# Optimization experiments

Measured on AMD Instinct MI355X. Metric: run time of the kernel, lower is better.

## Reference

```python
import jax, jax.numpy as jnp
import numpy as np

WINDOW_SIZE = 11
VAL_RANGE = 1.0
N_CHANNEL = 3
MS_WEIGHTS = jnp.array([0.0448, 0.2856, 0.3001, 0.2363, 0.1333], dtype=jnp.float32)


def _gaussian_window(window_size, sigma, channel):
    x = jnp.arange(window_size, dtype=jnp.float32)
    g = jnp.exp(-((x - window_size // 2) ** 2) / (2.0 * sigma ** 2))
    g = g / jnp.sum(g)
    w2d = jnp.outer(g, g)  # [ws, ws]
    # depthwise kernel in OIHW with feature_group_count=channel: [C, 1, ws, ws]
    return jnp.broadcast_to(w2d[None, None], (channel, 1, window_size, window_size))


def _dwconv(x, kernel):
    # x: [B, C, H, W], kernel: [C, 1, ws, ws], valid padding, groups=C
    return jax.lax.conv_general_dilated(
        x, kernel, window_strides=(1, 1), padding='VALID',
        dimension_numbers=('NCHW', 'OIHW', 'NCHW'),
        feature_group_count=kernel.shape[0])


def _avg_pool2(x):
    # kernel 2, stride 2, no padding (floor mode)
    s = jax.lax.reduce_window(x, 0.0, jax.lax.add,
                              (1, 1, 2, 2), (1, 1, 2, 2), 'VALID')
    return s * 0.25


def setup_inputs() -> dict:
    key = jax.random.key(0)
    k1, k2 = jax.random.split(key)
    output = jax.random.uniform(k1, (16, 3, 512, 512), dtype=jnp.float32)
    target = jax.random.uniform(k2, (16, 3, 512, 512), dtype=jnp.float32)
    return {"output": output, "target": target}


def reference(output, target):
    window = _gaussian_window(WINDOW_SIZE, 1.5, N_CHANNEL)
    L = VAL_RANGE
    C1 = (0.01 * L) ** 2
    C2 = (0.03 * L) ** 2
    cs_list, ssim_list = [], []
    for _ in range(MS_WEIGHTS.shape[0]):
        mu1 = _dwconv(output, window)
        mu2 = _dwconv(target, window)
        sigma1_sq = _dwconv(output * output, window) - mu1 * mu1
        sigma2_sq = _dwconv(target * target, window) - mu2 * mu2
        sigma12 = _dwconv(output * target, window) - mu1 * mu2
        denom = sigma1_sq + sigma2_sq + C2
        cs = (2.0 * sigma12 + C2) / denom
        ssim = (2.0 * mu1 * mu2 + C1) * (2.0 * sigma12 + C2) / (
            (mu1 * mu1 + mu2 * mu2 + C1) * denom)
        cs_list.append(jax.nn.relu(jnp.mean(cs)))
        ssim_list.append(jax.nn.relu(jnp.mean(ssim)))
        output = _avg_pool2(output)
        target = _avg_pool2(target)
    cs = (jnp.stack(cs_list) + 1.0) / 2.0
    ssim = (jnp.stack(ssim_list) + 1.0) / 2.0
    ms_ssim = jnp.prod((cs ** MS_WEIGHTS)[:-1]) * (ssim ** MS_WEIGHTS)[-1]
    return 1.0 - ms_ssim
```

## Files before the change

### kernel.cpp

```cpp
#include <hip/hip_runtime.h>

#define HALO 10
#define NIMG 48

#define GWLIST { 0.0010284f, 0.0075987f, 0.0360008f, 0.1093607f, 0.2130056f, \
                 0.2660117f, 0.2130056f, 0.1093607f, 0.0360008f, 0.0075987f, 0.0010284f }

#define PP   56
#define PSZ  (48 * 56)
#define HT0  (2 * PSZ)
#define HTP  56
#define HTSZ (32 * 56)
#define WT0  (HT0 + 5 * HTSZ)
#define LDSH (WT0 + 64 * 8)

typedef _Float16 half8 __attribute__((ext_vector_type(8)));
typedef _Float16 half4 __attribute__((ext_vector_type(4)));
typedef float    floatx4 __attribute__((ext_vector_type(4)));

template <bool FUSE>
__global__ __launch_bounds__(256, 5) void ssim_mfma_kernel(
    const float* __restrict__ A, const float* __restrict__ B,
    int H, int W, float2* __restrict__ partial,
    float* __restrict__ poolA, float* __restrict__ poolB)
{
    __shared__ __align__(16) _Float16 sm[LDSH];
    __shared__ float red[16];

    const float w[11] = GWLIST;
    const int tid  = threadIdx.x;
    const int lane = tid & 63;
    const int wv   = tid >> 6;
    const int gx0  = blockIdx.x * 32;
    const int gy0  = blockIdx.y * 32;
    const int z    = blockIdx.z;
    const float* a = A + (size_t)z * H * W;
    const float* b = B + (size_t)z * H * W;

    if (tid < 64) {
        int base = ((tid >> 4) << 3) - (tid & 15);
        half8 wf;
        #pragma unroll
        for (int i = 0; i < 8; ++i) {
            int j = base + i;
            float v = 0.f;
            #pragma unroll
            for (int J = 0; J < 11; ++J) v = (j == J) ? w[J] : v;
            wf[i] = (_Float16)v;
        }
        *(half8*)&sm[WT0 + tid * 8] = wf;
    }

    const bool fast = (gy0 + 48 <= H) && (gx0 + 48 <= W);
    for (int e = tid; e < 288; e += 256) {
        int r = e / 6, c8 = e - r * 6;
        float fa[8], fb[8];
        if (fast) {
            const float* pa = a + (size_t)(gy0 + r) * W + gx0 + c8 * 8;
            const float* pb = b + (size_t)(gy0 + r) * W + gx0 + c8 * 8;
            *(float4*)&fa[0] = *(const float4*)pa;
            *(float4*)&fa[4] = *(const float4*)(pa + 4);
            *(float4*)&fb[0] = *(const float4*)pb;
            *(float4*)&fb[4] = *(const float4*)(pb + 4);
        } else {
            int gy = gy0 + r;
            #pragma unroll
            for (int i = 0; i < 8; ++i) {
                int gx = gx0 + c8 * 8 + i;
                bool ok = (gy < H) && (gx < W);
                size_t idx = (size_t)gy * W + gx;
                fa[i] = ok ? a[idx] : 0.f;
                fb[i] = ok ? b[idx] : 0.f;
            }
        }
        half8 ha, hb;
        #pragma unroll
        for (int i = 0; i < 8; ++i) {
            ha[i] = (_Float16)fa[i];
            hb[i] = (_Float16)fb[i];
        }
        int o = r * PP + c8 * 8;
        *(half8*)&sm[o]       = ha;
        *(half8*)&sm[o + PSZ] = hb;
    }
    __syncthreads();

    const half8 wfrag = *(const half8*)&sm[WT0 + lane * 8];

    {
        const int arow = (lane & 15) * PP + ((lane >> 4) << 3);
        const int crow = (lane & 15) * HTP + ((lane >> 4) << 2);
        #pragma unroll 2
        for (int p = wv; p < 6; p += 4) {
            int m0 = (p >> 1) << 4;
            int x0 = (p & 1) << 4;
            int fb_ = m0 * PP + x0 + arow;
            half8 ha  = *(const half8*)&sm[fb_];
            half8 hb  = *(const half8*)&sm[fb_ + PSZ];
            half8 faa = ha * ha;
            half8 fbb = hb * hb;
            half8 fab = ha * hb;
            floatx4 zero = {0.f, 0.f, 0.f, 0.f};
            floatx4 c0 = __builtin_amdgcn_mfma_f32_16x16x32_f16(ha,  wfrag, zero, 0, 0, 0);
            floatx4 c1 = __builtin_amdgcn_mfma_f32_16x16x32_f16(hb,  wfrag, zero, 0, 0, 0);
            floatx4 c2 = __builtin_amdgcn_mfma_f32_16x16x32_f16(faa, wfrag, zero, 0, 0, 0);
            floatx4 c3 = __builtin_amdgcn_mfma_f32_16x16x32_f16(fbb, wfrag, zero, 0, 0, 0);
            floatx4 c4 = __builtin_amdgcn_mfma_f32_16x16x32_f16(fab, wfrag, zero, 0, 0, 0);
            int cb = HT0 + x0 * HTP + m0 + crow;
            half4 h0, h1, h2, h3, h4;
            #pragma unroll
            for (int i = 0; i < 4; ++i) {
                h0[i] = (_Float16)c0[i];
                h1[i] = (_Float16)c1[i];
                h2[i] = (_Float16)c2[i];
                h3[i] = (_Float16)c3[i];
                h4[i] = (_Float16)c4[i];
            }
            *(half4*)&sm[cb + 0 * HTSZ] = h0;
            *(half4*)&sm[cb + 1 * HTSZ] = h1;
            *(half4*)&sm[cb + 2 * HTSZ] = h2;
            *(half4*)&sm[cb + 3 * HTSZ] = h3;
            *(half4*)&sm[cb + 4 * HTSZ] = h4;
        }
    }
    __syncthreads();

    float csSum = 0.f, ssimSum = 0.f;
    {
        const int y0 = (wv >> 1) << 4;
        const int x0 = (wv & 1) << 4;
        const int brow = (lane & 15) * HTP + ((lane >> 4) << 3);
        floatx4 m[5];
        #pragma unroll
        for (int q = 0; q < 5; ++q) {
            half8 bfrag = *(const half8*)&sm[HT0 + q * HTSZ + x0 * HTP + y0 + brow];
            floatx4 c = {0.f, 0.f, 0.f, 0.f};
            m[q] = __builtin_amdgcn_mfma_f32_16x16x32_f16(wfrag, bfrag, c, 0, 0, 0);
        }
        const int OH = H - HALO, OW = W - HALO;
        const int gx  = gx0 + x0 + (lane & 15);
        const int gyb = gy0 + y0 + ((lane >> 4) << 2);
        const float C1 = 1e-4f;
        const float C2 = 9e-4f;
        if (gx < OW) {
            #pragma unroll
            for (int i = 0; i < 4; ++i) {
                int gy = gyb + i;
                if (gy < OH) {
                    float mu1 = m[0][i], mu2 = m[1][i];
                    float s1sq = m[2][i] - mu1 * mu1;
                    float s2sq = m[3][i] - mu2 * mu2;
                    float s12  = m[4][i] - mu1 * mu2;
                    float denom = s1sq + s2sq + C2;
                    float num   = 2.f * s12 + C2;
                    float csv = num * __frcp_rn(denom);
                    float ssv = csv * (2.f * mu1 * mu2 + C1) *
                                __frcp_rn(mu1 * mu1 + mu2 * mu2 + C1);
                    csSum   += csv;
                    ssimSum += ssv;
                }
            }
        }
    }

    #pragma unroll
    for (int off = 32; off > 0; off >>= 1) {
        csSum   += __shfl_down(csSum, off, 64);
        ssimSum += __shfl_down(ssimSum, off, 64);
    }
    if (lane == 0) {
        red[wv]     = csSum;
        red[8 + wv] = ssimSum;
    }
    __syncthreads();
    if (tid == 0) {
        float c = 0.f, s = 0.f;
        #pragma unroll
        for (int i = 0; i < 4; ++i) { c += red[i]; s += red[8 + i]; }
        int slot = (z * gridDim.y + blockIdx.y) * gridDim.x + blockIdx.x;
        partial[slot] = make_float2(c, s);
    }

    if (FUSE && tid < 128) {
        const int OH2 = H >> 1, OW2 = W >> 1;
        const int img = tid >> 6;
        const int rem = tid & 63;
        const int pr  = rem >> 2;
        const int pq  = rem & 3;
        const float* src = img ? b : a;
        float* dst = (img ? poolB : poolA) + (size_t)z * OH2 * OW2;
        size_t base = (size_t)(gy0 + 2 * pr) * W + gx0 + pq * 8;
        float4 r0 = *(const float4*)(src + base);
        float4 r1 = *(const float4*)(src + base + 4);
        float4 r2 = *(const float4*)(src + base + W);
        float4 r3 = *(const float4*)(src + base + W + 4);
        float4 o;
        o.x = 0.25f * (r0.x + r0.y + r2.x + r2.y);
        o.y = 0.25f * (r0.z + r0.w + r2.z + r2.w);
        o.z = 0.25f * (r1.x + r1.y + r3.x + r3.y);
        o.w = 0.25f * (r1.z + r1.w + r3.z + r3.w);
        *(float4*)(dst + (size_t)((gy0 >> 1) + pr) * OW2 + (gx0 >> 1) + pq * 4) = o;
    }
}

#define TH   32
#define ROWS (TH + HALO)
#define HSTR 32
#define HQ   (ROWS * HSTR)

template <bool FUSE>
__global__ __launch_bounds__(256, 5) void ssim_scalar_kernel(
    const float* __restrict__ A, const float* __restrict__ B,
    int H, int W, float2* __restrict__ partial,
    float* __restrict__ poolA, float* __restrict__ poolB)
{
    __shared__ __align__(16) float lds[5 * HQ];
    __shared__ float red[16];

    const float w[11] = GWLIST;

    const int tid = threadIdx.x;
    const int gx0 = blockIdx.x * 32;
    const int gy0 = blockIdx.y * TH;
    const int z   = blockIdx.z;
    const float* a = A + (size_t)z * H * W;
    const float* b = B + (size_t)z * H * W;

    const bool fast = (gy0 + ROWS <= H) && (gx0 + 44 <= W);
    for (int e = tid; e < ROWS * 8; e += 256) {
        int r = e >> 3, c0 = (e & 7) * 4;
        int gy = gy0 + r;
        float s1[4]  = {0.f, 0.f, 0.f, 0.f};
        float s2[4]  = {0.f, 0.f, 0.f, 0.f};
        float s11[4] = {0.f, 0.f, 0.f, 0.f};
        float s22[4] = {0.f, 0.f, 0.f, 0.f};
        float s12[4] = {0.f, 0.f, 0.f, 0.f};
        #pragma unroll
        for (int c = 0; c < 4; ++c) {
            float ea[4], eb[4];
            if (fast) {
                const float* pa = a + (size_t)gy * W + gx0 + c0 + 4 * c;
                const float* pb = b + (size_t)gy * W + gx0 + c0 + 4 * c;
                *(float4*)&ea[0] = *(const float4*)pa;
                *(float4*)&eb[0] = *(const float4*)pb;
            } else {
                #pragma unroll
                for (int t = 0; t < 4; ++t) {
                    int gx = gx0 + c0 + 4 * c + t;
                    bool ok = (gy < H) && (gx < W);
                    size_t idx = (size_t)gy * W + gx;
                    ea[t] = ok ? a[idx] : 0.f;
                    eb[t] = ok ? b[idx] : 0.f;
                }
            }
            #pragma unroll
            for (int mm = 0; mm < 4; ++mm) {
                const int i = 4 * c + mm;
                float va = ea[mm], vb = eb[mm];
                float vaa = va * va, vbb = vb * vb, vab = va * vb;
                #pragma unroll
                for (int k = 0; k < 4; ++k) {
                    const int j = i - k;
                    if (j >= 0 && j <= 10) {
                        float wj = w[j];
                        s1[k]  += wj * va;
                        s2[k]  += wj * vb;
                        s11[k] += wj * vaa;
                        s22[k] += wj * vbb;
                        s12[k] += wj * vab;
                    }
                }
            }
        }
        int hb = r * HSTR + c0;
        *(float4*)&lds[hb + 0 * HQ] = make_float4(s1[0],  s1[1],  s1[2],  s1[3]);
        *(float4*)&lds[hb + 1 * HQ] = make_float4(s2[0],  s2[1],  s2[2],  s2[3]);
        *(float4*)&lds[hb + 2 * HQ] = make_float4(s11[0], s11[1], s11[2], s11[3]);
        *(float4*)&lds[hb + 3 * HQ] = make_float4(s22[0], s22[1], s22[2], s22[3]);
        *(float4*)&lds[hb + 4 * HQ] = make_float4(s12[0], s12[1], s12[2], s12[3]);
    }
    __syncthreads();

    const float C1 = 1e-4f;
    const float C2 = 9e-4f;
    float csSum = 0.f, ssimSum = 0.f;
    {
        const int ox  = tid & 31;
        const int oy0 = (tid >> 5) * 4;
        float m[5][4];
        #pragma unroll
        for (int q = 0; q < 5; ++q) {
            const float* hq = &lds[q * HQ + oy0 * HSTR + ox];
            float win[14];
            #pragma unroll
            for (int i = 0; i < 14; ++i) win[i] = hq[i * HSTR];
            #pragma unroll
            for (int k = 0; k < 4; ++k) {
                float acc = 0.f;
                #pragma unroll
                for (int j = 0; j < 11; ++j) acc += w[j] * win[k + j];
                m[q][k] = acc;
            }
        }
        const int OH = H - HALO, OW = W - HALO;
        const int gx = gx0 + ox;
        #pragma unroll
        for (int k = 0; k < 4; ++k) {
            int gy = gy0 + oy0 + k;
            if (gy < OH && gx < OW) {
                float mu1 = m[0][k], mu2 = m[1][k];
                float s1sq = m[2][k] - mu1 * mu1;
                float s2sq = m[3][k] - mu2 * mu2;
                float s12  = m[4][k] - mu1 * mu2;
                float denom  = s1sq + s2sq + C2;
                float num_cs = 2.f * s12 + C2;
                float csv = num_cs * __frcp_rn(denom);
                float ssv = csv * (2.f * mu1 * mu2 + C1) *
                            __frcp_rn(mu1 * mu1 + mu2 * mu2 + C1);
                csSum   += csv;
                ssimSum += ssv;
            }
        }
    }

    #pragma unroll
    for (int off = 32; off > 0; off >>= 1) {
        csSum   += __shfl_down(csSum, off, 64);
        ssimSum += __shfl_down(ssimSum, off, 64);
    }
    int wave = tid >> 6, lane = tid & 63;
    if (lane == 0) {
        red[wave]     = csSum;
        red[8 + wave] = ssimSum;
    }
    __syncthreads();
    if (tid == 0) {
        float c = 0.f, s = 0.f;
        #pragma unroll
        for (int i = 0; i < 4; ++i) { c += red[i]; s += red[8 + i]; }
        int slot = (z * gridDim.y + blockIdx.y) * gridDim.x + blockIdx.x;
        partial[slot] = make_float2(c, s);
    }

    if (FUSE && tid < 128) {
        const int OH2 = H >> 1, OW2 = W >> 1;
        const int img = tid >> 6;
        const int rem = tid & 63;
        const int pr  = rem >> 2;
        const int pq  = rem & 3;
        const float* src = img ? b : a;
        float* dst = (img ? poolB : poolA) + (size_t)z * OH2 * OW2;
        size_t base = (size_t)(gy0 + 2 * pr) * W + gx0 + pq * 8;
        float4 r0 = *(const float4*)(src + base);
        float4 r1 = *(const float4*)(src + base + 4);
        float4 r2 = *(const float4*)(src + base + W);
        float4 r3 = *(const float4*)(src + base + W + 4);
        float4 o;
        o.x = 0.25f * (r0.x + r0.y + r2.x + r2.y);
        o.y = 0.25f * (r0.z + r0.w + r2.z + r2.w);
        o.z = 0.25f * (r1.x + r1.y + r3.x + r3.y);
        o.w = 0.25f * (r1.z + r1.w + r3.z + r3.w);
        *(float4*)(dst + (size_t)((gy0 >> 1) + pr) * OW2 + (gx0 >> 1) + pq * 4) = o;
    }
}

__global__ void final_kernel(const float2* __restrict__ partial, float* __restrict__ out) {
    __shared__ double red[8];
    __shared__ double resC[5], resS[5];
    const int segs[6] = {0, 12288, 15360, 16128, 16320, 16368};
    const int tid = threadIdx.x;
    for (int s = 0; s < 5; ++s) {
        double c = 0.0, v = 0.0;
        #pragma unroll 4
        for (int i = segs[s] + tid; i < segs[s + 1]; i += 256) {
            float2 p = partial[i];
            c += (double)p.x;
            v += (double)p.y;
        }
        #pragma unroll
        for (int off = 32; off > 0; off >>= 1) {
            c += __shfl_down(c, off, 64);
            v += __shfl_down(v, off, 64);
        }
        int wave = tid >> 6, lane = tid & 63;
        __syncthreads();
        if (lane == 0) { red[wave] = c; red[4 + wave] = v; }
        __syncthreads();
        if (tid == 0) {
            resC[s] = red[0] + red[1] + red[2] + red[3];
            resS[s] = red[4] + red[5] + red[6] + red[7];
        }
    }
    __syncthreads();
    if (tid == 0) {
        const double wgt[5] = {0.0448, 0.2856, 0.3001, 0.2363, 0.1333};
        double ms = 1.0;
        for (int s = 0; s < 5; ++s) {
            int Hs = 512 >> s;
            double cnt = (double)NIMG * (double)(Hs - 10) * (double)(Hs - 10);
            double cs = resC[s] / cnt;
            double sv = resS[s] / cnt;
            if (cs < 0.0) cs = 0.0;
            if (sv < 0.0) sv = 0.0;
            cs = (cs + 1.0) * 0.5;
            sv = (sv + 1.0) * 0.5;
            ms *= pow((s < 4) ? cs : sv, wgt[s]);
        }
        out[0] = (float)(1.0 - ms);
    }
}

extern "C" void kernel_launch(void* const* d_in, const int* in_sizes, int n_in,
                              void* d_out, int out_size, void* d_ws, size_t ws_size,
                              hipStream_t stream) {
    (void)in_sizes; (void)n_in; (void)out_size; (void)ws_size;
    const float* A0 = (const float*)d_in[0];
    const float* B0 = (const float*)d_in[1];
    float* out = (float*)d_out;

    char* ws = (char*)d_ws;
    float2* partial = (float2*)ws;
    float* pyr = (float*)(ws + (1 << 18));

    float* pa[5] = {nullptr, nullptr, nullptr, nullptr, nullptr};
    float* pb[5] = {nullptr, nullptr, nullptr, nullptr, nullptr};
    size_t off = 0;
    for (int s = 1; s <= 4; ++s) {
        int Hs = 512 >> s;
        size_t n = (size_t)NIMG * Hs * Hs;
        pa[s] = pyr + off; off += n;
        pb[s] = pyr + off; off += n;
    }

    const int segs[5] = {0, 12288, 15360, 16128, 16320};

    const float* curA = A0;
    const float* curB = B0;
    for (int s = 0; s < 5; ++s) {
        int Hs = 512 >> s;
        int g  = Hs >> 5;
        dim3 grid(g, g, NIMG);
        if (s < 2) {
            ssim_mfma_kernel<true><<<grid, 256, 0, stream>>>(
                curA, curB, Hs, Hs, partial + segs[s], pa[s + 1], pb[s + 1]);
            curA = pa[s + 1];
            curB = pb[s + 1];
        } else if (s < 4) {
            ssim_scalar_kernel<true><<<grid, 256, 0, stream>>>(
                curA, curB, Hs, Hs, partial + segs[s], pa[s + 1], pb[s + 1]);
            curA = pa[s + 1];
            curB = pb[s + 1];
        } else {
            ssim_scalar_kernel<false><<<grid, 256, 0, stream>>>(
                curA, curB, Hs, Hs, partial + segs[s], nullptr, nullptr);
        }
    }

    final_kernel<<<1, 256, 0, stream>>>(partial, out);
}
```

Baseline: 208.7 us.

## Process two tiles per block and prefetch second tile during first compute

```diff
diff --git a/kernel.cpp b/kernel.cpp
--- a/kernel.cpp
+++ b/kernel.cpp
@@ -18,151 +18,140 @@
 typedef _Float16 half4 __attribute__((ext_vector_type(4)));
 typedef float    floatx4 __attribute__((ext_vector_type(4)));
 
-template <bool FUSE>
-__global__ __launch_bounds__(256, 5) void ssim_mfma_kernel(
-    const float* __restrict__ A, const float* __restrict__ B,
-    int H, int W, float2* __restrict__ partial,
-    float* __restrict__ poolA, float* __restrict__ poolB)
-{
-    __shared__ __align__(16) _Float16 sm[LDSH];
-    __shared__ float red[16];
-
-    const float w[11] = GWLIST;
-    const int tid  = threadIdx.x;
-    const int lane = tid & 63;
-    const int wv   = tid >> 6;
-    const int gx0  = blockIdx.x * 32;
-    const int gy0  = blockIdx.y * 32;
-    const int z    = blockIdx.z;
-    const float* a = A + (size_t)z * H * W;
-    const float* b = B + (size_t)z * H * W;
-
-    if (tid < 64) {
-        int base = ((tid >> 4) << 3) - (tid & 15);
-        half8 wf;
+struct JR { float4 al, ah, bl, bh; };
+
+__device__ __forceinline__ void issue_job(const float* __restrict__ a,
+                                          const float* __restrict__ b,
+                                          int H, int W, int gx0, int gy0,
+                                          int e, bool fast, JR& r)
+{
+    int rr = e / 6, c8 = e - rr * 6;
+    if (fast) {
+        const float* pa = a + (size_t)(gy0 + rr) * W + gx0 + c8 * 8;
+        const float* pb = b + (size_t)(gy0 + rr) * W + gx0 + c8 * 8;
+        r.al = *(const float4*)pa;       r.ah = *(const float4*)(pa + 4);
+        r.bl = *(const float4*)pb;       r.bh = *(const float4*)(pb + 4);
+    } else {
+        float fa[8], fb[8];
+        int gy = gy0 + rr;
         #pragma unroll
         for (int i = 0; i < 8; ++i) {
-            int j = base + i;
-            float v = 0.f;
-            #pragma unroll
-            for (int J = 0; J < 11; ++J) v = (j == J) ? w[J] : v;
-            wf[i] = (_Float16)v;
-        }
-        *(half8*)&sm[WT0 + tid * 8] = wf;
-    }
-
-    const bool fast = (gy0 + 48 <= H) && (gx0 + 48 <= W);
-    for (int e = tid; e < 288; e += 256) {
-        int r = e / 6, c8 = e - r * 6;
-        float fa[8], fb[8];
-        if (fast) {
-            const float* pa = a + (size_t)(gy0 + r) * W + gx0 + c8 * 8;
-            const float* pb = b + (size_t)(gy0 + r) * W + gx0 + c8 * 8;
-            *(float4*)&fa[0] = *(const float4*)pa;
-            *(float4*)&fa[4] = *(const float4*)(pa + 4);
-            *(float4*)&fb[0] = *(const float4*)pb;
-            *(float4*)&fb[4] = *(const float4*)(pb + 4);
-        } else {
-            int gy = gy0 + r;
-            #pragma unroll
-            for (int i = 0; i < 8; ++i) {
-                int gx = gx0 + c8 * 8 + i;
-                bool ok = (gy < H) && (gx < W);
-                size_t idx = (size_t)gy * W + gx;
-                fa[i] = ok ? a[idx] : 0.f;
-                fb[i] = ok ? b[idx] : 0.f;
+            int gx = gx0 + c8 * 8 + i;
+            bool ok = (gy < H) && (gx < W);
+            size_t idx = (size_t)gy * W + gx;
+            fa[i] = ok ? a[idx] : 0.f;
+            fb[i] = ok ? b[idx] : 0.f;
+        }
+        r.al = make_float4(fa[0], fa[1], fa[2], fa[3]);
+        r.ah = make_float4(fa[4], fa[5], fa[6], fa[7]);
+        r.bl = make_float4(fb[0], fb[1], fb[2], fb[3]);
+        r.bh = make_float4(fb[4], fb[5], fb[6], fb[7]);
+    }
+}
+
+__device__ __forceinline__ void store_job(_Float16* __restrict__ sm, int e, const JR& r)
+{
+    int rr = e / 6, c8 = e - rr * 6;
+    float fa[8] = {r.al.x, r.al.y, r.al.z, r.al.w, r.ah.x, r.ah.y, r.ah.z, r.ah.w};
+    float fb[8] = {r.bl.x, r.bl.y, r.bl.z, r.bl.w, r.bh.x, r.bh.y, r.bh.z, r.bh.w};
+    half8 ha, hb;
+    #pragma unroll
+    for (int i = 0; i < 8; ++i) {
+        ha[i] = (_Float16)fa[i];
+        hb[i] = (_Float16)fb[i];
+    }
+    int o = rr * PP + c8 * 8;
+    *(half8*)&sm[o]       = ha;
+    *(half8*)&sm[o + PSZ] = hb;
+}
+
+__device__ __forceinline__ void stage2(_Float16* __restrict__ sm, half8 wfrag,
+                                       int lane, int wv)
+{
+    const int arow = (lane & 15) * PP + ((lane >> 4) << 3);
+    const int crow = (lane & 15) * HTP + ((lane >> 4) << 2);
+    #pragma unroll 2
+    for (int p = wv; p < 6; p += 4) {
+        int m0 = (p >> 1) << 4;
+        int x0 = (p & 1) << 4;
+        int fb_ = m0 * PP + x0 + arow;
+        half8 ha  = *(const half8*)&sm[fb_];
+        half8 hb  = *(const half8*)&sm[fb_ + PSZ];
+        half8 faa = ha * ha;
+        half8 fbb = hb * hb;
+        half8 fab = ha * hb;
+        floatx4 zero = {0.f, 0.f, 0.f, 0.f};
+        floatx4 c0 = __builtin_amdgcn_mfma_f32_16x16x32_f16(ha,  wfrag, zero, 0, 0, 0);
+        floatx4 c1 = __builtin_amdgcn_mfma_f32_16x16x32_f16(hb,  wfrag, zero, 0, 0, 0);
+        floatx4 c2 = __builtin_amdgcn_mfma_f32_16x16x32_f16(faa, wfrag, zero, 0, 0, 0);
+        floatx4 c3 = __builtin_amdgcn_mfma_f32_16x16x32_f16(fbb, wfrag, zero, 0, 0, 0);
+        floatx4 c4 = __builtin_amdgcn_mfma_f32_16x16x32_f16(fab, wfrag, zero, 0, 0, 0);
+        int cb = HT0 + x0 * HTP + m0 + crow;
+        half4 h0, h1, h2, h3, h4;
+        #pragma unroll
+        for (int i = 0; i < 4; ++i) {
+            h0[i] = (_Float16)c0[i];
+            h1[i] = (_Float16)c1[i];
+            h2[i] = (_Float16)c2[i];
+            h3[i] = (_Float16)c3[i];
+            h4[i] = (_Float16)c4[i];
+        }
+        *(half4*)&sm[cb + 0 * HTSZ] = h0;
+        *(half4*)&sm[cb + 1 * HTSZ] = h1;
+        *(half4*)&sm[cb + 2 * HTSZ] = h2;
+        *(half4*)&sm[cb + 3 * HTSZ] = h3;
+        *(half4*)&sm[cb + 4 * HTSZ] = h4;
+    }
+}
+
+__device__ __forceinline__ void stage3(const _Float16* __restrict__ sm, half8 wfrag,
+                                       int lane, int wv, int H, int W,
+                                       int gx0, int gy0,
+                                       float& csSum, float& ssimSum)
+{
+    const int y0 = (wv >> 1) << 4;
+    const int x0 = (wv & 1) << 4;
+    const int brow = (lane & 15) * HTP + ((lane >> 4) << 3);
+    floatx4 m[5];
+    #pragma unroll
+    for (int q = 0; q < 5; ++q) {
+        half8 bfrag = *(const half8*)&sm[HT0 + q * HTSZ + x0 * HTP + y0 + brow];
+        floatx4 c = {0.f, 0.f, 0.f, 0.f};
+        m[q] = __builtin_amdgcn_mfma_f32_16x16x32_f16(wfrag, bfrag, c, 0, 0, 0);
+    }
+    const int OH = H - HALO, OW = W - HALO;
+    const int gx  = gx0 + x0 + (lane & 15);
+    const int gyb = gy0 + y0 + ((lane >> 4) << 2);
+    const float C1 = 1e-4f;
+    const float C2 = 9e-4f;
+    csSum = 0.f; ssimSum = 0.f;
+    if (gx < OW) {
+        #pragma unroll
+        for (int i = 0; i < 4; ++i) {
+            int gy = gyb + i;
+            if (gy < OH) {
+                float mu1 = m[0][i], mu2 = m[1][i];
+                float s1sq = m[2][i] - mu1 * mu1;
+                float s2sq = m[3][i] - mu2 * mu2;
+                float s12  = m[4][i] - mu1 * mu2;
+                float denom = s1sq + s2sq + C2;
+                float num   = 2.f * s12 + C2;
+                float csv = num * __frcp_rn(denom);
+                float ssv = csv * (2.f * mu1 * mu2 + C1) *
+                            __frcp_rn(mu1 * mu1 + mu2 * mu2 + C1);
+                csSum   += csv;
+                ssimSum += ssv;
             }
         }
-        half8 ha, hb;
-        #pragma unroll
-        for (int i = 0; i < 8; ++i) {
-            ha[i] = (_Float16)fa[i];
-            hb[i] = (_Float16)fb[i];
-        }
-        int o = r * PP + c8 * 8;
-        *(half8*)&sm[o]       = ha;
-        *(half8*)&sm[o + PSZ] = hb;
-    }
-    __syncthreads();
-
-    const half8 wfrag = *(const half8*)&sm[WT0 + lane * 8];
-
-    {
-        const int arow = (lane & 15) * PP + ((lane >> 4) << 3);
-        const int crow = (lane & 15) * HTP + ((lane >> 4) << 2);
-        #pragma unroll 2
-        for (int p = wv; p < 6; p += 4) {
-            int m0 = (p >> 1) << 4;
-            int x0 = (p & 1) << 4;
-            int fb_ = m0 * PP + x0 + arow;
-            half8 ha  = *(const half8*)&sm[fb_];
-            half8 hb  = *(const half8*)&sm[fb_ + PSZ];
-            half8 faa = ha * ha;
-            half8 fbb = hb * hb;
-            half8 fab = ha * hb;
-            floatx4 zero = {0.f, 0.f, 0.f, 0.f};
-            floatx4 c0 = __builtin_amdgcn_mfma_f32_16x16x32_f16(ha,  wfrag, zero, 0, 0, 0);
-            floatx4 c1 = __builtin_amdgcn_mfma_f32_16x16x32_f16(hb,  wfrag, zero, 0, 0, 0);
-            floatx4 c2 = __builtin_amdgcn_mfma_f32_16x16x32_f16(faa, wfrag, zero, 0, 0, 0);
-            floatx4 c3 = __builtin_amdgcn_mfma_f32_16x16x32_f16(fbb, wfrag, zero, 0, 0, 0);
-            floatx4 c4 = __builtin_amdgcn_mfma_f32_16x16x32_f16(fab, wfrag, zero, 0, 0, 0);
-            int cb = HT0 + x0 * HTP + m0 + crow;
-            half4 h0, h1, h2, h3, h4;
-            #pragma unroll
-            for (int i = 0; i < 4; ++i) {
-                h0[i] = (_Float16)c0[i];
-                h1[i] = (_Float16)c1[i];
-                h2[i] = (_Float16)c2[i];
-                h3[i] = (_Float16)c3[i];
-                h4[i] = (_Float16)c4[i];
-            }
-            *(half4*)&sm[cb + 0 * HTSZ] = h0;
-            *(half4*)&sm[cb + 1 * HTSZ] = h1;
-            *(half4*)&sm[cb + 2 * HTSZ] = h2;
-            *(half4*)&sm[cb + 3 * HTSZ] = h3;
-            *(half4*)&sm[cb + 4 * HTSZ] = h4;
-        }
-    }
-    __syncthreads();
-
-    float csSum = 0.f, ssimSum = 0.f;
-    {
-        const int y0 = (wv >> 1) << 4;
-        const int x0 = (wv & 1) << 4;
-        const int brow = (lane & 15) * HTP + ((lane >> 4) << 3);
-        floatx4 m[5];
-        #pragma unroll
-        for (int q = 0; q < 5; ++q) {
-            half8 bfrag = *(const half8*)&sm[HT0 + q * HTSZ + x0 * HTP + y0 + brow];
-            floatx4 c = {0.f, 0.f, 0.f, 0.f};
-            m[q] = __builtin_amdgcn_mfma_f32_16x16x32_f16(wfrag, bfrag, c, 0, 0, 0);
-        }
-        const int OH = H - HALO, OW = W - HALO;
-        const int gx  = gx0 + x0 + (lane & 15);
-        const int gyb = gy0 + y0 + ((lane >> 4) << 2);
-        const float C1 = 1e-4f;
-        const float C2 = 9e-4f;
-        if (gx < OW) {
-            #pragma unroll
-            for (int i = 0; i < 4; ++i) {
-                int gy = gyb + i;
-                if (gy < OH) {
-                    float mu1 = m[0][i], mu2 = m[1][i];
-                    float s1sq = m[2][i] - mu1 * mu1;
-                    float s2sq = m[3][i] - mu2 * mu2;
-                    float s12  = m[4][i] - mu1 * mu2;
-                    float denom = s1sq + s2sq + C2;
-                    float num   = 2.f * s12 + C2;
-                    float csv = num * __frcp_rn(denom);
-                    float ssv = csv * (2.f * mu1 * mu2 + C1) *
-                                __frcp_rn(mu1 * mu1 + mu2 * mu2 + C1);
-                    csSum   += csv;
-                    ssimSum += ssv;
-                }
-            }
-        }
-    }
-
+    }
+}
+
+__device__ __forceinline__ void block_reduce_store(float csSum, float ssimSum,
+                                                   float* __restrict__ red,
+                                                   int tid, int lane, int wv,
+                                                   float2* __restrict__ partial,
+                                                   int slot)
+{
     #pragma unroll
     for (int off = 32; off > 0; off >>= 1) {
         csSum   += __shfl_down(csSum, off, 64);
@@ -177,11 +166,17 @@
         float c = 0.f, s = 0.f;
         #pragma unroll
         for (int i = 0; i < 4; ++i) { c += red[i]; s += red[8 + i]; }
-        int slot = (z * gridDim.y + blockIdx.y) * gridDim.x + blockIdx.x;
         partial[slot] = make_float2(c, s);
     }
-
-    if (FUSE && tid < 128) {
+}
+
+__device__ __forceinline__ void pool_tile(const float* __restrict__ a,
+                                          const float* __restrict__ b,
+                                          int H, int W, int gx0, int gy0, int z,
+                                          float* __restrict__ poolA,
+                                          float* __restrict__ poolB, int tid)
+{
+    if (tid < 128) {
         const int OH2 = H >> 1, OW2 = W >> 1;
         const int img = tid >> 6;
         const int rem = tid & 63;
@@ -201,6 +196,87 @@
         o.w = 0.25f * (r1.z + r1.w + r3.z + r3.w);
         *(float4*)(dst + (size_t)((gy0 >> 1) + pr) * OW2 + (gx0 >> 1) + pq * 4) = o;
     }
+}
+
+template <bool FUSE>
+__global__ __launch_bounds__(256, 5) void ssim_mfma_kernel(
+    const float* __restrict__ A, const float* __restrict__ B,
+    int H, int W, float2* __restrict__ partial,
+    float* __restrict__ poolA, float* __restrict__ poolB)
+{
+    __shared__ __align__(16) _Float16 sm[LDSH];
+    __shared__ float red[16];
+
+    const float w[11] = GWLIST;
+    const int tid  = threadIdx.x;
+    const int lane = tid & 63;
+    const int wv   = tid >> 6;
+    const int tx0  = blockIdx.x * 2;
+    const int gxA  = tx0 * 32;
+    const int gxB  = gxA + 32;
+    const int gy0  = blockIdx.y * 32;
+    const int z    = blockIdx.z;
+    const float* a = A + (size_t)z * H * W;
+    const float* b = B + (size_t)z * H * W;
+
+    const int tilesX = gridDim.x * 2;
+    const int slotA  = (z * gridDim.y + blockIdx.y) * tilesX + tx0;
+
+    const bool fastA = (gy0 + 48 <= H) && (gxA + 48 <= W);
+    const bool fastB = (gy0 + 48 <= H) && (gxB + 48 <= W);
+    const int  e0 = tid;
+    const int  e1 = tid + 256;
+    const bool has2 = (tid < 32);
+
+    JR j0, j1;
+    issue_job(a, b, H, W, gxA, gy0, e0, fastA, j0);
+    if (has2) issue_job(a, b, H, W, gxA, gy0, e1, fastA, j1);
+
+    if (tid < 64) {
+        int base = ((tid >> 4) << 3) - (tid & 15);
+        half8 wf;
+        #pragma unroll
+        for (int i = 0; i < 8; ++i) {
+            int j = base + i;
+            float v = 0.f;
+            #pragma unroll
+            for (int J = 0; J < 11; ++J) v = (j == J) ? w[J] : v;
+            wf[i] = (_Float16)v;
+        }
+        *(half8*)&sm[WT0 + tid * 8] = wf;
+    }
+
+    store_job(sm, e0, j0);
+    if (has2) store_job(sm, e1, j1);
+    __syncthreads();
+
+    const half8 wfrag = *(const half8*)&sm[WT0 + lane * 8];
+
+    JR k0, k1;
+    issue_job(a, b, H, W, gxB, gy0, e0, fastB, k0);
+    if (has2) issue_job(a, b, H, W, gxB, gy0, e1, fastB, k1);
+
+    stage2(sm, wfrag, lane, wv);
+    __syncthreads();
+
+    float cs0, ss0;
+    stage3(sm, wfrag, lane, wv, H, W, gxA, gy0, cs0, ss0);
+
+    store_job(sm, e0, k0);
+    if (has2) store_job(sm, e1, k1);
+
+    block_reduce_store(cs0, ss0, red, tid, lane, wv, partial, slotA);
+
+    if (FUSE) pool_tile(a, b, H, W, gxA, gy0, z, poolA, poolB, tid);
+
+    stage2(sm, wfrag, lane, wv);
+    __syncthreads();
+
+    float cs1, ss1;
+    stage3(sm, wfrag, lane, wv, H, W, gxB, gy0, cs1, ss1);
+    block_reduce_store(cs1, ss1, red, tid, lane, wv, partial, slotA + 1);
+
+    if (FUSE) pool_tile(a, b, H, W, gxB, gy0, z, poolA, poolB, tid);
 }
 
 #define TH   32
@@ -439,18 +515,20 @@
     for (int s = 0; s < 5; ++s) {
         int Hs = 512 >> s;
         int g  = Hs >> 5;
-        dim3 grid(g, g, NIMG);
         if (s < 2) {
+            dim3 grid(g >> 1, g, NIMG);
             ssim_mfma_kernel<true><<<grid, 256, 0, stream>>>(
                 curA, curB, Hs, Hs, partial + segs[s], pa[s + 1], pb[s + 1]);
             curA = pa[s + 1];
             curB = pb[s + 1];
         } else if (s < 4) {
+            dim3 grid(g, g, NIMG);
             ssim_scalar_kernel<true><<<grid, 256, 0, stream>>>(
                 curA, curB, Hs, Hs, partial + segs[s], pa[s + 1], pb[s + 1]);
             curA = pa[s + 1];
             curB = pb[s + 1];
         } else {
+            dim3 grid(g, g, NIMG);
             ssim_scalar_kernel<false><<<grid, 256, 0, stream>>>(
                 curA, curB, Hs, Hs, partial + segs[s], nullptr, nullptr);
         }
```

Result: no change. 211.0 us (+1.1%).

## Alias horizontal-pass buffer onto input patch to shrink LDS and raise occupancy

Applied to the files above, without the earlier changes.

```diff
diff --git a/kernel.cpp b/kernel.cpp
--- a/kernel.cpp
+++ b/kernel.cpp
@@ -8,18 +8,56 @@
 
 #define PP   56
 #define PSZ  (48 * 56)
-#define HT0  (2 * PSZ)
 #define HTP  56
 #define HTSZ (32 * 56)
-#define WT0  (HT0 + 5 * HTSZ)
+#define WT0  (5 * HTSZ)
 #define LDSH (WT0 + 64 * 8)
 
 typedef _Float16 half8 __attribute__((ext_vector_type(8)));
 typedef _Float16 half4 __attribute__((ext_vector_type(4)));
 typedef float    floatx4 __attribute__((ext_vector_type(4)));
 
+__device__ __forceinline__ void hconv_pos(const _Float16* __restrict__ sm,
+                                          half8 wfrag, int p, int arow,
+                                          half4 out[5])
+{
+    int m0 = (p >> 1) << 4;
+    int x0 = (p & 1) << 4;
+    int fb_ = m0 * PP + x0 + arow;
+    half8 ha  = *(const half8*)&sm[fb_];
+    half8 hb  = *(const half8*)&sm[fb_ + PSZ];
+    half8 faa = ha * ha;
+    half8 fbb = hb * hb;
+    half8 fab = ha * hb;
+    floatx4 zero = {0.f, 0.f, 0.f, 0.f};
+    floatx4 c0 = __builtin_amdgcn_mfma_f32_16x16x32_f16(ha,  wfrag, zero, 0, 0, 0);
+    floatx4 c1 = __builtin_amdgcn_mfma_f32_16x16x32_f16(hb,  wfrag, zero, 0, 0, 0);
+    floatx4 c2 = __builtin_amdgcn_mfma_f32_16x16x32_f16(faa, wfrag, zero, 0, 0, 0);
+    floatx4 c3 = __builtin_amdgcn_mfma_f32_16x16x32_f16(fbb, wfrag, zero, 0, 0, 0);
+    floatx4 c4 = __builtin_amdgcn_mfma_f32_16x16x32_f16(fab, wfrag, zero, 0, 0, 0);
+    #pragma unroll
+    for (int i = 0; i < 4; ++i) {
+        out[0][i] = (_Float16)c0[i];
+        out[1][i] = (_Float16)c1[i];
+        out[2][i] = (_Float16)c2[i];
+        out[3][i] = (_Float16)c3[i];
+        out[4][i] = (_Float16)c4[i];
+    }
+}
+
+__device__ __forceinline__ void hwrite_pos(_Float16* __restrict__ sm,
+                                           int p, int crow, const half4 out[5])
+{
+    int m0 = (p >> 1) << 4;
+    int x0 = (p & 1) << 4;
+    int cb = x0 * HTP + m0 + crow;
+    #pragma unroll
+    for (int q = 0; q < 5; ++q)
+        *(half4*)&sm[cb + q * HTSZ] = out[q];
+}
+
 template <bool FUSE>
-__global__ __launch_bounds__(256, 5) void ssim_mfma_kernel(
+__global__ __launch_bounds__(256, 7) void ssim_mfma_kernel(
     const float* __restrict__ A, const float* __restrict__ B,
     int H, int W, float2* __restrict__ partial,
     float* __restrict__ poolA, float* __restrict__ poolB)
@@ -87,41 +125,19 @@
 
     const half8 wfrag = *(const half8*)&sm[WT0 + lane * 8];
 
+    half4 r0[5], r1[5];
+    const bool have1 = (wv < 2);
     {
         const int arow = (lane & 15) * PP + ((lane >> 4) << 3);
+        hconv_pos(sm, wfrag, wv, arow, r0);
+        if (have1) hconv_pos(sm, wfrag, wv + 4, arow, r1);
+    }
+    __syncthreads();
+
+    {
         const int crow = (lane & 15) * HTP + ((lane >> 4) << 2);
-        #pragma unroll 2
-        for (int p = wv; p < 6; p += 4) {
-            int m0 = (p >> 1) << 4;
-            int x0 = (p & 1) << 4;
-            int fb_ = m0 * PP + x0 + arow;
-            half8 ha  = *(const half8*)&sm[fb_];
-            half8 hb  = *(const half8*)&sm[fb_ + PSZ];
-            half8 faa = ha * ha;
-            half8 fbb = hb * hb;
-            half8 fab = ha * hb;
-            floatx4 zero = {0.f, 0.f, 0.f, 0.f};
-            floatx4 c0 = __builtin_amdgcn_mfma_f32_16x16x32_f16(ha,  wfrag, zero, 0, 0, 0);
-            floatx4 c1 = __builtin_amdgcn_mfma_f32_16x16x32_f16(hb,  wfrag, zero, 0, 0, 0);
-            floatx4 c2 = __builtin_amdgcn_mfma_f32_16x16x32_f16(faa, wfrag, zero, 0, 0, 0);
-            floatx4 c3 = __builtin_amdgcn_mfma_f32_16x16x32_f16(fbb, wfrag, zero, 0, 0, 0);
-            floatx4 c4 = __builtin_amdgcn_mfma_f32_16x16x32_f16(fab, wfrag, zero, 0, 0, 0);
-            int cb = HT0 + x0 * HTP + m0 + crow;
-            half4 h0, h1, h2, h3, h4;
-            #pragma unroll
-            for (int i = 0; i < 4; ++i) {
-                h0[i] = (_Float16)c0[i];
-                h1[i] = (_Float16)c1[i];
-                h2[i] = (_Float16)c2[i];
-                h3[i] = (_Float16)c3[i];
-                h4[i] = (_Float16)c4[i];
-            }
-            *(half4*)&sm[cb + 0 * HTSZ] = h0;
-            *(half4*)&sm[cb + 1 * HTSZ] = h1;
-            *(half4*)&sm[cb + 2 * HTSZ] = h2;
-            *(half4*)&sm[cb + 3 * HTSZ] = h3;
-            *(half4*)&sm[cb + 4 * HTSZ] = h4;
-        }
+        hwrite_pos(sm, wv, crow, r0);
+        if (have1) hwrite_pos(sm, wv + 4, crow, r1);
     }
     __syncthreads();
 
@@ -133,7 +149,7 @@
         floatx4 m[5];
         #pragma unroll
         for (int q = 0; q < 5; ++q) {
-            half8 bfrag = *(const half8*)&sm[HT0 + q * HTSZ + x0 * HTP + y0 + brow];
+            half8 bfrag = *(const half8*)&sm[q * HTSZ + x0 * HTP + y0 + brow];
             floatx4 c = {0.f, 0.f, 0.f, 0.f};
             m[q] = __builtin_amdgcn_mfma_f32_16x16x32_f16(wfrag, bfrag, c, 0, 0, 0);
         }
@@ -171,6 +187,167 @@
     if (lane == 0) {
         red[wv]     = csSum;
         red[8 + wv] = ssimSum;
+    }
+    __syncthreads();
+    if (tid == 0) {
+        float c = 0.f, s = 0.f;
+        #pragma unroll
+        for (int i = 0; i < 4; ++i) { c += red[i]; s += red[8 + i]; }
+        int slot = (z * gridDim.y + blockIdx.y) * gridDim.x + blockIdx.x;
+        partial[slot] = make_float2(c, s);
+    }
+
+    if (FUSE && tid < 128) {
+        const int OH2 = H >> 1, OW2 = W >> 1;
+        const int img = tid >> 6;
+        const int rem = tid & 63;
+        const int pr  = rem >> 2;
+        const int pq  = rem & 3;
+        const float* src = img ? b : a;
+        float* dst = (img ? poolB : poolA) + (size_t)z * OH2 * OW2;
+        size_t base = (size_t)(gy0 + 2 * pr) * W + gx0 + pq * 8;
+        float4 r0v = *(const float4*)(src + base);
+        float4 r1v = *(const float4*)(src + base + 4);
+        float4 r2v = *(const float4*)(src + base + W);
+        float4 r3v = *(const float4*)(src + base + W + 4);
+        float4 o;
+        o.x = 0.25f * (r0v.x + r0v.y + r2v.x + r2v.y);
+        o.y = 0.25f * (r0v.z + r0v.w + r2v.z + r2v.w);
+        o.z = 0.25f * (r1v.x + r1v.y + r3v.x + r3v.y);
+        o.w = 0.25f * (r1v.z + r1v.w + r3v.z + r3v.w);
+        *(float4*)(dst + (size_t)((gy0 >> 1) + pr) * OW2 + (gx0 >> 1) + pq * 4) = o;
+    }
+}
+
+#define TH   32
+#define ROWS (TH + HALO)
+#define HSTR 32
+#define HQ   (ROWS * HSTR)
+
+template <bool FUSE>
+__global__ __launch_bounds__(256, 5) void ssim_scalar_kernel(
+    const float* __restrict__ A, const float* __restrict__ B,
+    int H, int W, float2* __restrict__ partial,
+    float* __restrict__ poolA, float* __restrict__ poolB)
+{
+    __shared__ __align__(16) float lds[5 * HQ];
+    __shared__ float red[16];
+
+    const float w[11] = GWLIST;
+
+    const int tid = threadIdx.x;
+    const int gx0 = blockIdx.x * 32;
+    const int gy0 = blockIdx.y * TH;
+    const int z   = blockIdx.z;
+    const float* a = A + (size_t)z * H * W;
+    const float* b = B + (size_t)z * H * W;
+
+    const bool fast = (gy0 + ROWS <= H) && (gx0 + 44 <= W);
+    for (int e = tid; e < ROWS * 8; e += 256) {
+        int r = e >> 3, c0 = (e & 7) * 4;
+        int gy = gy0 + r;
+        float s1[4]  = {0.f, 0.f, 0.f, 0.f};
+        float s2[4]  = {0.f, 0.f, 0.f, 0.f};
+        float s11[4] = {0.f, 0.f, 0.f, 0.f};
+        float s22[4] = {0.f, 0.f, 0.f, 0.f};
+        float s12[4] = {0.f, 0.f, 0.f, 0.f};
+        #pragma unroll
+        for (int c = 0; c < 4; ++c) {
+            float ea[4], eb[4];
+            if (fast) {
+                const float* pa = a + (size_t)gy * W + gx0 + c0 + 4 * c;
+                const float* pb = b + (size_t)gy * W + gx0 + c0 + 4 * c;
+                *(float4*)&ea[0] = *(const float4*)pa;
+                *(float4*)&eb[0] = *(const float4*)pb;
+            } else {
+                #pragma unroll
+                for (int t = 0; t < 4; ++t) {
+                    int gx = gx0 + c0 + 4 * c + t;
+                    bool ok = (gy < H) && (gx < W);
+                    size_t idx = (size_t)gy * W + gx;
+                    ea[t] = ok ? a[idx] : 0.f;
+                    eb[t] = ok ? b[idx] : 0.f;
+                }
+            }
+            #pragma unroll
+            for (int mm = 0; mm < 4; ++mm) {
+                const int i = 4 * c + mm;
+                float va = ea[mm], vb = eb[mm];
+                float vaa = va * va, vbb = vb * vb, vab = va * vb;
+                #pragma unroll
+                for (int k = 0; k < 4; ++k) {
+                    const int j = i - k;
+                    if (j >= 0 && j <= 10) {
+                        float wj = w[j];
+                        s1[k]  += wj * va;
+                        s2[k]  += wj * vb;
+                        s11[k] += wj * vaa;
+                        s22[k] += wj * vbb;
+                        s12[k] += wj * vab;
+                    }
+                }
+            }
+        }
+        int hb = r * HSTR + c0;
+        *(float4*)&lds[hb + 0 * HQ] = make_float4(s1[0],  s1[1],  s1[2],  s1[3]);
+        *(float4*)&lds[hb + 1 * HQ] = make_float4(s2[0],  s2[1],  s2[2],  s2[3]);
+        *(float4*)&lds[hb + 2 * HQ] = make_float4(s11[0], s11[1], s11[2], s11[3]);
+        *(float4*)&lds[hb + 3 * HQ] = make_float4(s22[0], s22[1], s22[2], s22[3]);
+        *(float4*)&lds[hb + 4 * HQ] = make_float4(s12[0], s12[1], s12[2], s12[3]);
+    }
+    __syncthreads();
+
+    const float C1 = 1e-4f;
+    const float C2 = 9e-4f;
+    float csSum = 0.f, ssimSum = 0.f;
+    {
+        const int ox  = tid & 31;
+        const int oy0 = (tid >> 5) * 4;
+        float m[5][4];
+        #pragma unroll
+        for (int q = 0; q < 5; ++q) {
+            const float* hq = &lds[q * HQ + oy0 * HSTR + ox];
+            float win[14];
+            #pragma unroll
+            for (int i = 0; i < 14; ++i) win[i] = hq[i * HSTR];
+            #pragma unroll
+            for (int k = 0; k < 4; ++k) {
+                float acc = 0.f;
+                #pragma unroll
+                for (int j = 0; j < 11; ++j) acc += w[j] * win[k + j];
+                m[q][k] = acc;
+            }
+        }
+        const int OH = H - HALO, OW = W - HALO;
+        const int gx = gx0 + ox;
+        #pragma unroll
+        for (int k = 0; k < 4; ++k) {
+            int gy = gy0 + oy0 + k;
+            if (gy < OH && gx < OW) {
+                float mu1 = m[0][k], mu2 = m[1][k];
+                float s1sq = m[2][k] - mu1 * mu1;
+                float s2sq = m[3][k] - mu2 * mu2;
+                float s12  = m[4][k] - mu1 * mu2;
+                float denom  = s1sq + s2sq + C2;
+                float num_cs = 2.f * s12 + C2;
+                float csv = num_cs * __frcp_rn(denom);
+                float ssv = csv * (2.f * mu1 * mu2 + C1) *
+                            __frcp_rn(mu1 * mu1 + mu2 * mu2 + C1);
+                csSum   += csv;
+                ssimSum += ssv;
+            }
+        }
+    }
+
+    #pragma unroll
+    for (int off = 32; off > 0; off >>= 1) {
+        csSum   += __shfl_down(csSum, off, 64);
+        ssimSum += __shfl_down(ssimSum, off, 64);
+    }
+    int wave = tid >> 6, lane = tid & 63;
+    if (lane == 0) {
+        red[wave]     = csSum;
+        red[8 + wave] = ssimSum;
     }
     __syncthreads();
     if (tid == 0) {
@@ -203,167 +380,6 @@
     }
 }
 
-#define TH   32
-#define ROWS (TH + HALO)
-#define HSTR 32
-#define HQ   (ROWS * HSTR)
-
-template <bool FUSE>
-__global__ __launch_bounds__(256, 5) void ssim_scalar_kernel(
-    const float* __restrict__ A, const float* __restrict__ B,
-    int H, int W, float2* __restrict__ partial,
-    float* __restrict__ poolA, float* __restrict__ poolB)
-{
-    __shared__ __align__(16) float lds[5 * HQ];
-    __shared__ float red[16];
-
-    const float w[11] = GWLIST;
-
-    const int tid = threadIdx.x;
-    const int gx0 = blockIdx.x * 32;
-    const int gy0 = blockIdx.y * TH;
-    const int z   = blockIdx.z;
-    const float* a = A + (size_t)z * H * W;
-    const float* b = B + (size_t)z * H * W;
-
-    const bool fast = (gy0 + ROWS <= H) && (gx0 + 44 <= W);
-    for (int e = tid; e < ROWS * 8; e += 256) {
-        int r = e >> 3, c0 = (e & 7) * 4;
-        int gy = gy0 + r;
-        float s1[4]  = {0.f, 0.f, 0.f, 0.f};
-        float s2[4]  = {0.f, 0.f, 0.f, 0.f};
-        float s11[4] = {0.f, 0.f, 0.f, 0.f};
-        float s22[4] = {0.f, 0.f, 0.f, 0.f};
-        float s12[4] = {0.f, 0.f, 0.f, 0.f};
-        #pragma unroll
-        for (int c = 0; c < 4; ++c) {
-            float ea[4], eb[4];
-            if (fast) {
-                const float* pa = a + (size_t)gy * W + gx0 + c0 + 4 * c;
-                const float* pb = b + (size_t)gy * W + gx0 + c0 + 4 * c;
-                *(float4*)&ea[0] = *(const float4*)pa;
-                *(float4*)&eb[0] = *(const float4*)pb;
-            } else {
-                #pragma unroll
-                for (int t = 0; t < 4; ++t) {
-                    int gx = gx0 + c0 + 4 * c + t;
-                    bool ok = (gy < H) && (gx < W);
-                    size_t idx = (size_t)gy * W + gx;
-                    ea[t] = ok ? a[idx] : 0.f;
-                    eb[t] = ok ? b[idx] : 0.f;
-                }
-            }
-            #pragma unroll
-            for (int mm = 0; mm < 4; ++mm) {
-                const int i = 4 * c + mm;
-                float va = ea[mm], vb = eb[mm];
-                float vaa = va * va, vbb = vb * vb, vab = va * vb;
-                #pragma unroll
-                for (int k = 0; k < 4; ++k) {
-                    const int j = i - k;
-                    if (j >= 0 && j <= 10) {
-                        float wj = w[j];
-                        s1[k]  += wj * va;
-                        s2[k]  += wj * vb;
-                        s11[k] += wj * vaa;
-                        s22[k] += wj * vbb;
-                        s12[k] += wj * vab;
-                    }
-                }
-            }
-        }
-        int hb = r * HSTR + c0;
-        *(float4*)&lds[hb + 0 * HQ] = make_float4(s1[0],  s1[1],  s1[2],  s1[3]);
-        *(float4*)&lds[hb + 1 * HQ] = make_float4(s2[0],  s2[1],  s2[2],  s2[3]);
-        *(float4*)&lds[hb + 2 * HQ] = make_float4(s11[0], s11[1], s11[2], s11[3]);
-        *(float4*)&lds[hb + 3 * HQ] = make_float4(s22[0], s22[1], s22[2], s22[3]);
-        *(float4*)&lds[hb + 4 * HQ] = make_float4(s12[0], s12[1], s12[2], s12[3]);
-    }
-    __syncthreads();
-
-    const float C1 = 1e-4f;
-    const float C2 = 9e-4f;
-    float csSum = 0.f, ssimSum = 0.f;
-    {
-        const int ox  = tid & 31;
-        const int oy0 = (tid >> 5) * 4;
-        float m[5][4];
-        #pragma unroll
-        for (int q = 0; q < 5; ++q) {
-            const float* hq = &lds[q * HQ + oy0 * HSTR + ox];
-            float win[14];
-            #pragma unroll
-            for (int i = 0; i < 14; ++i) win[i] = hq[i * HSTR];
-            #pragma unroll
-            for (int k = 0; k < 4; ++k) {
-                float acc = 0.f;
-                #pragma unroll
-                for (int j = 0; j < 11; ++j) acc += w[j] * win[k + j];
-                m[q][k] = acc;
-            }
-        }
-        const int OH = H - HALO, OW = W - HALO;
-        const int gx = gx0 + ox;
-        #pragma unroll
-        for (int k = 0; k < 4; ++k) {
-            int gy = gy0 + oy0 + k;
-            if (gy < OH && gx < OW) {
-                float mu1 = m[0][k], mu2 = m[1][k];
-                float s1sq = m[2][k] - mu1 * mu1;
-                float s2sq = m[3][k] - mu2 * mu2;
-                float s12  = m[4][k] - mu1 * mu2;
-                float denom  = s1sq + s2sq + C2;
-                float num_cs = 2.f * s12 + C2;
-                float csv = num_cs * __frcp_rn(denom);
-                float ssv = csv * (2.f * mu1 * mu2 + C1) *
-                            __frcp_rn(mu1 * mu1 + mu2 * mu2 + C1);
-                csSum   += csv;
-                ssimSum += ssv;
-            }
-        }
-    }
-
-    #pragma unroll
-    for (int off = 32; off > 0; off >>= 1) {
-        csSum   += __shfl_down(csSum, off, 64);
-        ssimSum += __shfl_down(ssimSum, off, 64);
-    }
-    int wave = tid >> 6, lane = tid & 63;
-    if (lane == 0) {
-        red[wave]     = csSum;
-        red[8 + wave] = ssimSum;
-    }
-    __syncthreads();
-    if (tid == 0) {
-        float c = 0.f, s = 0.f;
-        #pragma unroll
-        for (int i = 0; i < 4; ++i) { c += red[i]; s += red[8 + i]; }
-        int slot = (z * gridDim.y + blockIdx.y) * gridDim.x + blockIdx.x;
-        partial[slot] = make_float2(c, s);
-    }
-
-    if (FUSE && tid < 128) {
-        const int OH2 = H >> 1, OW2 = W >> 1;
-        const int img = tid >> 6;
-        const int rem = tid & 63;
-        const int pr  = rem >> 2;
-        const int pq  = rem & 3;
-        const float* src = img ? b : a;
-        float* dst = (img ? poolB : poolA) + (size_t)z * OH2 * OW2;
-        size_t base = (size_t)(gy0 + 2 * pr) * W + gx0 + pq * 8;
-        float4 r0 = *(const float4*)(src + base);
-        float4 r1 = *(const float4*)(src + base + 4);
-        float4 r2 = *(const float4*)(src + base + W);
-        float4 r3 = *(const float4*)(src + base + W + 4);
-        float4 o;
-        o.x = 0.25f * (r0.x + r0.y + r2.x + r2.y);
-        o.y = 0.25f * (r0.z + r0.w + r2.z + r2.w);
-        o.z = 0.25f * (r1.x + r1.y + r3.x + r3.y);
-        o.w = 0.25f * (r1.z + r1.w + r3.z + r3.w);
-        *(float4*)(dst + (size_t)((gy0 >> 1) + pr) * OW2 + (gx0 >> 1) + pq * 4) = o;
-    }
-}
-
 __global__ void final_kernel(const float2* __restrict__ partial, float* __restrict__ out) {
     __shared__ double red[8];
     __shared__ double resC[5], resS[5];
```

Result: faster. 200.3 us (-4.0%).
